# Kernel optimization log

Measured on AMD Instinct MI355X. Metric: run time of the kernel, lower is better.

The kernel has to match this reference:

```python
import jax, jax.numpy as jnp
import numpy as np

N_NODES = 50000
N_EDGES = 800000
N_GRAPHS = 512
IN_DIM = 256
HID = 512
N_CLASSES = 10
BN_EPS = 1e-5


def setup_inputs() -> dict:
    key = jax.random.key(0)
    ks = jax.random.split(key, 32)
    x = jax.random.normal(ks[0], (N_NODES, IN_DIM), dtype=jnp.float32)
    edge_index = jax.random.randint(ks[1], (2, N_EDGES), 0, N_NODES, dtype=jnp.int64)
    batch = jnp.sort(jax.random.randint(ks[2], (N_NODES,), 0, N_GRAPHS, dtype=jnp.int64))

    def lin(k, fan_in, fan_out):
        kw, kb = jax.random.split(k)
        s = 1.0 / np.sqrt(fan_in)
        w = jax.random.uniform(kw, (fan_in, fan_out), jnp.float32, -s, s)
        b = jax.random.uniform(kb, (fan_out,), jnp.float32, -s, s)
        return w, b

    inp = {"x": x, "edge_index": edge_index, "batch": batch}
    # GIN layer 0 MLP (in->hid->hid), layers 1,2 (hid->hid->hid)
    inp["w0a"], inp["b0a"] = lin(ks[3], IN_DIM, HID)
    inp["w0b"], inp["b0b"] = lin(ks[4], HID, HID)
    inp["w1a"], inp["b1a"] = lin(ks[5], HID, HID)
    inp["w1b"], inp["b1b"] = lin(ks[6], HID, HID)
    inp["w2a"], inp["b2a"] = lin(ks[7], HID, HID)
    inp["w2b"], inp["b2b"] = lin(ks[8], HID, HID)
    # BatchNorm affine params
    for i in range(3):
        inp[f"bn{i}_g"] = jnp.ones((HID,), jnp.float32)
        inp[f"bn{i}_b"] = jnp.zeros((HID,), jnp.float32)
    # classifier
    inp["clf_w1"], inp["clf_b1"] = lin(ks[9], HID, HID)
    inp["clf_w2"], inp["clf_b2"] = lin(ks[10], HID, N_CLASSES)
    return inp


def _gin_layer(h, src, dst, wa, ba, wb, bb, g, b):
    # sum-aggregate neighbors (source -> target), eps = 0 (PyG default)
    agg = jax.ops.segment_sum(h[src], dst, num_segments=N_NODES)
    z = h + agg
    # 2-layer MLP: Linear -> ReLU -> Linear
    z = jax.nn.relu(z @ wa + ba) @ wb + bb
    # BatchNorm1d with batch statistics (training mode, biased var) + affine
    mu = jnp.mean(z, axis=0)
    var = jnp.var(z, axis=0)
    z = (z - mu) * jax.lax.rsqrt(var + BN_EPS) * g + b
    return jax.nn.relu(z)


def reference(x, edge_index, batch,
              w0a, b0a, w0b, b0b,
              w1a, b1a, w1b, b1b,
              w2a, b2a, w2b, b2b,
              bn0_g, bn0_b, bn1_g, bn1_b, bn2_g, bn2_b,
              clf_w1, clf_b1, clf_w2, clf_b2):
    src, dst = edge_index[0], edge_index[1]
    h = _gin_layer(x, src, dst, w0a, b0a, w0b, b0b, bn0_g, bn0_b)
    h = _gin_layer(h, src, dst, w1a, b1a, w1b, b1b, bn1_g, bn1_b)
    h = _gin_layer(h, src, dst, w2a, b2a, w2b, b2b, bn2_g, bn2_b)
    # global add pool over graphs
    gpool = jax.ops.segment_sum(h, batch, num_segments=N_GRAPHS)  # [G, HID]
    # classifier (dropout = identity in eval)
    logits = jax.nn.relu(gpool @ clf_w1 + clf_b1) @ clf_w2 + clf_b2
    probs = jax.nn.softmax(logits, axis=1)
    preds = jnp.argmax(probs, axis=1)
    one_hot = jax.nn.one_hot(preds, N_CLASSES, dtype=logits.dtype)
    return (logits, probs, preds.astype(jnp.float32), one_hot)
```

## Files before the change

kernel.cpp:

```cpp
#include <hip/hip_runtime.h>

#define N_NODES 50000
#define N_EDGES 800000
#define N_GRAPHS 512
#define IN_DIM 256
#define HID 512
#define BN_EPS 1e-5f

typedef __attribute__((ext_vector_type(8))) short bf16x8;
typedef __attribute__((ext_vector_type(4))) float f32x4;

__device__ inline void split_bf16(float a, unsigned short& hi, unsigned short& lo) {
  unsigned u = __float_as_uint(a);
  hi = (unsigned short)(u >> 16);
  float fh = __uint_as_float(u & 0xFFFF0000u);
  float r = a - fh;
  lo = (unsigned short)(__float_as_uint(r) >> 16);
}

__device__ inline void split4_store(float4 v, unsigned short* hip, unsigned short* lop) {
  unsigned short h0, h1, h2, h3, l0, l1, l2, l3;
  split_bf16(v.x, h0, l0);
  split_bf16(v.y, h1, l1);
  split_bf16(v.z, h2, l2);
  split_bf16(v.w, h3, l3);
  uint2 hv, lv;
  hv.x = (unsigned)h0 | ((unsigned)h1 << 16);
  hv.y = (unsigned)h2 | ((unsigned)h3 << 16);
  lv.x = (unsigned)l0 | ((unsigned)l1 << 16);
  lv.y = (unsigned)l2 | ((unsigned)l3 << 16);
  *(uint2*)hip = hv;
  *(uint2*)lop = lv;
}

__device__ inline float4 bnrelu4(float4 v, float4 s, float4 h) {
  float4 o;
  o.x = fmaxf(fmaf(v.x, s.x, h.x), 0.f);
  o.y = fmaxf(fmaf(v.y, s.y, h.y), 0.f);
  o.z = fmaxf(fmaf(v.z, s.z, h.z), 0.f);
  o.w = fmaxf(fmaf(v.w, s.w, h.w), 0.f);
  return o;
}

__global__ __launch_bounds__(256) void hist_dst(const int* __restrict__ dst,
                                                int* __restrict__ deg) {
  for (int e = blockIdx.x * 256 + threadIdx.x; e < N_EDGES; e += gridDim.x * 256)
    atomicAdd(&deg[dst[e]], 1);
}

__global__ __launch_bounds__(1024) void scan_deg(const int* __restrict__ deg,
                                                 int* __restrict__ off,
                                                 int* __restrict__ cursor) {
  __shared__ int partial[1024];
  const int t = threadIdx.x;
  const int CHUNK = 49;
  const int base = t * CHUNK;
  int mysum = 0;
  for (int i = 0; i < CHUNK; ++i) {
    int idx = base + i;
    if (idx < N_NODES) mysum += deg[idx];
  }
  partial[t] = mysum;
  __syncthreads();
  for (int st = 1; st < 1024; st <<= 1) {
    int v = (t >= st) ? partial[t - st] : 0;
    __syncthreads();
    partial[t] += v;
    __syncthreads();
  }
  int run = partial[t] - mysum;
  for (int i = 0; i < CHUNK; ++i) {
    int idx = base + i;
    if (idx < N_NODES) {
      off[idx] = run;
      cursor[idx] = run;
      run += deg[idx];
    }
  }
  if (t == 1023) off[N_NODES] = N_EDGES;
}

__global__ __launch_bounds__(256) void fill_csr(const int* __restrict__ src,
                                                const int* __restrict__ dst,
                                                int* __restrict__ cursor,
                                                int* __restrict__ eidx) {
  for (int e = blockIdx.x * 256 + threadIdx.x; e < N_EDGES; e += gridDim.x * 256) {
    int p = atomicAdd(&cursor[dst[e]], 1);
    eidx[p] = src[e];
  }
}

template <int ROWF4, int HASBN>
__global__ __launch_bounds__(256) void agg_pk(const float4* __restrict__ h4,
                                              const int* __restrict__ off,
                                              const int* __restrict__ eidx,
                                              const float4* __restrict__ scale4,
                                              const float4* __restrict__ shift4,
                                              unsigned short* __restrict__ zp) {
  const int n = blockIdx.x * 4 + (threadIdx.x >> 6);
  if (n >= N_NODES) return;
  const int lane = threadIdx.x & 63;
  const int ROW = ROWF4 * 64;
  float4 sc[ROWF4], sh[ROWF4];
  if (HASBN) {
#pragma unroll
    for (int j = 0; j < ROWF4; ++j) {
      sc[j] = scale4[j * 64 + lane];
      sh[j] = shift4[j * 64 + lane];
    }
  }
  float4 v[ROWF4];
  const float4* hn = h4 + (long long)n * ROW;
#pragma unroll
  for (int j = 0; j < ROWF4; ++j) {
    float4 a = hn[j * 64 + lane];
    v[j] = HASBN ? bnrelu4(a, sc[j], sh[j]) : a;
  }

  int p = off[n];
  const int pe = off[n + 1];
  for (; p + 4 <= pe; p += 4) {
    int s0 = eidx[p], s1 = eidx[p + 1], s2 = eidx[p + 2], s3 = eidx[p + 3];
    const float4* h0 = h4 + (long long)s0 * ROW;
    const float4* h1 = h4 + (long long)s1 * ROW;
    const float4* h2 = h4 + (long long)s2 * ROW;
    const float4* h3 = h4 + (long long)s3 * ROW;
#pragma unroll
    for (int j = 0; j < ROWF4; ++j) {
      float4 a = h0[j * 64 + lane];
      float4 b = h1[j * 64 + lane];
      float4 c = h2[j * 64 + lane];
      float4 d = h3[j * 64 + lane];
      if (HASBN) {
        a = bnrelu4(a, sc[j], sh[j]);
        b = bnrelu4(b, sc[j], sh[j]);
        c = bnrelu4(c, sc[j], sh[j]);
        d = bnrelu4(d, sc[j], sh[j]);
      }
      v[j].x += (a.x + b.x) + (c.x + d.x);
      v[j].y += (a.y + b.y) + (c.y + d.y);
      v[j].z += (a.z + b.z) + (c.z + d.z);
      v[j].w += (a.w + b.w) + (c.w + d.w);
    }
  }
  for (; p < pe; ++p) {
    int s0 = eidx[p];
    const float4* h0 = h4 + (long long)s0 * ROW;
#pragma unroll
    for (int j = 0; j < ROWF4; ++j) {
      float4 a = h0[j * 64 + lane];
      if (HASBN) a = bnrelu4(a, sc[j], sh[j]);
      v[j].x += a.x;
      v[j].y += a.y;
      v[j].z += a.z;
      v[j].w += a.w;
    }
  }
  const int nd = n & 63, tile = n >> 6;
  const int nf = nd >> 4, ccs = nd & 15;
#pragma unroll
  for (int j = 0; j < ROWF4; ++j) {
    int cj = j * 64 + lane;
    int ks = cj >> 3, k4 = cj & 7;
    size_t base = ((size_t)tile * (ROWF4 * 8) + ks) * 4096 +
                  (size_t)nf * 512 + (size_t)(k4 >> 1) * 128 + (size_t)ccs * 8 +
                  (size_t)(k4 & 1) * 4;
    split4_store(v[j], zp + base, zp + base + 2048);
  }
}

__global__ __launch_bounds__(256) void wt_build(const float* __restrict__ W,
                                                unsigned short* __restrict__ Wp,
                                                int KS) {
  int gid = blockIdx.x * 256 + threadIdx.x;
  int total = 2 * KS * 8192;
  if (gid >= total) return;
  int blk = gid >> 13;
  int rem = gid & 8191;
  int cf = rem >> 9;
  int q = (rem >> 7) & 3;
  int c = (rem >> 3) & 15;
  int j = rem & 7;
  int bx = blk / KS, ks = blk - bx * KS;
  int chan = bx * 256 + cf * 16 + c;
  int k = ks * 32 + q * 8 + j;
  float v = W[(size_t)k * 512 + chan];
  unsigned short h, l;
  split_bf16(v, h, l);
  Wp[(size_t)blk * 16384 + rem] = h;
  Wp[(size_t)blk * 16384 + 8192 + rem] = l;
}

template <int STATS, int PACKOUT>
__global__ __launch_bounds__(256) void gemm_pk(const unsigned short* __restrict__ Ap,
                                               const unsigned short* __restrict__ Wp,
                                               const float* __restrict__ bias,
                                               float* __restrict__ Cf,
                                               unsigned short* __restrict__ Cp,
                                               float* __restrict__ stat_sum,
                                               float* __restrict__ stat_sq,
                                               int N, int KS, int relu) {
  const int tid = threadIdx.x;
  const int wv = tid >> 6, ln = tid & 63;
  const int bx = blockIdx.x;
  const int tile = blockIdx.y;
  const int n0 = tile * 64;

  f32x4 acc[4][4];
#pragma unroll
  for (int i = 0; i < 4; ++i)
#pragma unroll
    for (int j = 0; j < 4; ++j) acc[i][j] = f32x4{0.f, 0.f, 0.f, 0.f};

  const unsigned short* wp =
      Wp + ((size_t)bx * KS) * 16384 + (size_t)(wv * 4) * 512 + (size_t)ln * 8;
  const unsigned short* ap = Ap + (size_t)tile * KS * 4096 + (size_t)ln * 8;

  for (int ks = 0; ks < KS; ++ks) {
    const unsigned short* w = wp + (size_t)ks * 16384;
    const unsigned short* a = ap + (size_t)ks * 4096;
    bf16x8 wh[4], wl[4], ah[4], al[4];
#pragma unroll
    for (int i = 0; i < 4; ++i) {
      wh[i] = *(const bf16x8*)(w + i * 512);
      wl[i] = *(const bf16x8*)(w + 8192 + i * 512);
    }
#pragma unroll
    for (int j = 0; j < 4; ++j) {
      ah[j] = *(const bf16x8*)(a + j * 512);
      al[j] = *(const bf16x8*)(a + 2048 + j * 512);
    }
#pragma unroll
    for (int i = 0; i < 4; ++i)
#pragma unroll
      for (int j = 0; j < 4; ++j) {
        acc[i][j] = __builtin_amdgcn_mfma_f32_16x16x32_bf16(wh[i], ah[j], acc[i][j], 0, 0, 0);
        acc[i][j] = __builtin_amdgcn_mfma_f32_16x16x32_bf16(wh[i], al[j], acc[i][j], 0, 0, 0);
        acc[i][j] = __builtin_amdgcn_mfma_f32_16x16x32_bf16(wl[i], ah[j], acc[i][j], 0, 0, 0);
      }
  }

  const int chanb = bx * 256 + wv * 64 + (ln >> 4) * 4;
  float4 s4[4], q4[4];
  if (STATS) {
#pragma unroll
    for (int i = 0; i < 4; ++i) {
      s4[i] = make_float4(0.f, 0.f, 0.f, 0.f);
      q4[i] = make_float4(0.f, 0.f, 0.f, 0.f);
    }
  }
#pragma unroll
  for (int j = 0; j < 4; ++j) {
    int node = n0 + j * 16 + (ln & 15);
    bool valid = node < N;
    int nd = node & 63;
    int tile2 = node >> 6, nf = nd >> 4, ccs = nd & 15;
#pragma unroll
    for (int i = 0; i < 4; ++i) {
      int chan = chanb + i * 16;
      float4 bv = *(const float4*)(bias + chan);
      f32x4 a = acc[i][j];
      float4 o;
      o.x = a[0] + bv.x;
      o.y = a[1] + bv.y;
      o.z = a[2] + bv.z;
      o.w = a[3] + bv.w;
      if (relu) {
        o.x = fmaxf(o.x, 0.f);
        o.y = fmaxf(o.y, 0.f);
        o.z = fmaxf(o.z, 0.f);
        o.w = fmaxf(o.w, 0.f);
      }
      if (PACKOUT) {
        if (valid) {
          size_t base = ((size_t)tile2 * 16 + (size_t)(chan >> 5)) * 4096 +
                        (size_t)nf * 512 + (size_t)((chan >> 3) & 3) * 128 +
                        (size_t)ccs * 8 + (size_t)((chan >> 2) & 1) * 4;
          split4_store(o, Cp + base, Cp + base + 2048);
        }
      } else {
        if (valid) *(float4*)(Cf + (size_t)node * 512 + chan) = o;
        if (STATS) {
          if (!valid) o = make_float4(0.f, 0.f, 0.f, 0.f);
          s4[i].x += o.x; s4[i].y += o.y; s4[i].z += o.z; s4[i].w += o.w;
          q4[i].x += o.x * o.x; q4[i].y += o.y * o.y;
          q4[i].z += o.z * o.z; q4[i].w += o.w * o.w;
        }
      }
    }
  }
  if (STATS) {
#pragma unroll
    for (int i = 0; i < 4; ++i) {
#pragma unroll
      for (int mask = 1; mask < 16; mask <<= 1) {
        s4[i].x += __shfl_xor(s4[i].x, mask);
        s4[i].y += __shfl_xor(s4[i].y, mask);
        s4[i].z += __shfl_xor(s4[i].z, mask);
        s4[i].w += __shfl_xor(s4[i].w, mask);
        q4[i].x += __shfl_xor(q4[i].x, mask);
        q4[i].y += __shfl_xor(q4[i].y, mask);
        q4[i].z += __shfl_xor(q4[i].z, mask);
        q4[i].w += __shfl_xor(q4[i].w, mask);
      }
    }
    if ((ln & 15) == 0) {
#pragma unroll
      for (int i = 0; i < 4; ++i) {
        int chan = chanb + i * 16;
        atomicAdd(&stat_sum[chan + 0], s4[i].x);
        atomicAdd(&stat_sum[chan + 1], s4[i].y);
        atomicAdd(&stat_sum[chan + 2], s4[i].z);
        atomicAdd(&stat_sum[chan + 3], s4[i].w);
        atomicAdd(&stat_sq[chan + 0], q4[i].x);
        atomicAdd(&stat_sq[chan + 1], q4[i].y);
        atomicAdd(&stat_sq[chan + 2], q4[i].z);
        atomicAdd(&stat_sq[chan + 3], q4[i].w);
      }
    }
  }
}

__global__ __launch_bounds__(512) void bn_finalize(const float* __restrict__ sum,
                                                   const float* __restrict__ sumsq,
                                                   const float* __restrict__ g,
                                                   const float* __restrict__ b,
                                                   float* __restrict__ scale,
                                                   float* __restrict__ shift) {
  const int c = threadIdx.x;
  const float invN = 1.0f / (float)N_NODES;
  float mu = sum[c] * invN;
  float var = sumsq[c] * invN - mu * mu;
  float sc = rsqrtf(var + BN_EPS) * g[c];
  scale[c] = sc;
  shift[c] = fmaf(-mu, sc, b[c]);
}

__global__ __launch_bounds__(512) void pool_bounds(const int* __restrict__ batch,
                                                   int* __restrict__ gstart) {
  const int g = threadIdx.x;
  int lo = 0, hi = N_NODES;
  while (lo < hi) {
    int mid = (lo + hi) >> 1;
    if (batch[mid] < g) lo = mid + 1;
    else hi = mid;
  }
  gstart[g] = lo;
  if (g == 0) gstart[N_GRAPHS] = N_NODES;
}

__global__ __launch_bounds__(128) void gpool_bn(const float4* __restrict__ z4,
                                                const int* __restrict__ gstart,
                                                const float4* __restrict__ scale4,
                                                const float4* __restrict__ shift4,
                                                unsigned short* __restrict__ gpp) {
  const int g = blockIdx.x;
  const int t = threadIdx.x;
  const int s = gstart[g], e = gstart[g + 1];
  const float4 sc = scale4[t], sh = shift4[t];
  float4 acc = make_float4(0.f, 0.f, 0.f, 0.f);
  for (int n = s; n < e; ++n) {
    float4 v = bnrelu4(z4[(size_t)n * 128 + t], sc, sh);
    acc.x += v.x;
    acc.y += v.y;
    acc.z += v.z;
    acc.w += v.w;
  }
  const int tile = g >> 6, nd = g & 63;
  const int nf = nd >> 4, ccs = nd & 15;
  const int ks = t >> 3, k4 = t & 7;
  size_t base = ((size_t)tile * 16 + ks) * 4096 + (size_t)nf * 512 +
                (size_t)(k4 >> 1) * 128 + (size_t)ccs * 8 + (size_t)(k4 & 1) * 4;
  split4_store(acc, gpp + base, gpp + base + 2048);
}

__global__ __launch_bounds__(64) void clf2_softmax(const float* __restrict__ hidden,
                                                   const float* __restrict__ w2,
                                                   const float* __restrict__ b2,
                                                   float* __restrict__ out) {
  const int g = blockIdx.x;
  const int lane = threadIdx.x;
  float acc[10];
#pragma unroll
  for (int j = 0; j < 10; ++j) acc[j] = 0.f;
  for (int k = lane; k < HID; k += 64) {
    float hv = hidden[(long long)g * HID + k];
#pragma unroll
    for (int j = 0; j < 10; ++j) acc[j] += hv * w2[k * 10 + j];
  }
#pragma unroll
  for (int j = 0; j < 10; ++j) {
    for (int o = 32; o > 0; o >>= 1) acc[j] += __shfl_down(acc[j], o);
  }
  if (lane == 0) {
    float lg[10], pb[10];
    float mx = -1e30f;
#pragma unroll
    for (int j = 0; j < 10; ++j) {
      lg[j] = acc[j] + b2[j];
      mx = fmaxf(mx, lg[j]);
    }
    float se = 0.f;
#pragma unroll
    for (int j = 0; j < 10; ++j) {
      pb[j] = __expf(lg[j] - mx);
      se += pb[j];
    }
    float inv = 1.f / se;
    int am = 0;
    float best = lg[0];
#pragma unroll
    for (int j = 1; j < 10; ++j) {
      if (lg[j] > best) { best = lg[j]; am = j; }
    }
#pragma unroll
    for (int j = 0; j < 10; ++j) out[g * 10 + j] = lg[j];
#pragma unroll
    for (int j = 0; j < 10; ++j) out[N_GRAPHS * 10 + g * 10 + j] = pb[j] * inv;
    out[2 * N_GRAPHS * 10 + g] = (float)am;
#pragma unroll
    for (int j = 0; j < 10; ++j)
      out[2 * N_GRAPHS * 10 + N_GRAPHS + g * 10 + j] = (j == am) ? 1.f : 0.f;
  }
}

extern "C" void kernel_launch(void* const* d_in, const int* in_sizes, int n_in,
                              void* d_out, int out_size, void* d_ws, size_t ws_size,
                              hipStream_t stream) {
  const float* x = (const float*)d_in[0];
  const int* src = (const int*)d_in[1];
  const int* dstE = src + N_EDGES;
  const int* batch = (const int*)d_in[2];
  const float* w0a = (const float*)d_in[3];
  const float* b0a = (const float*)d_in[4];
  const float* w0b = (const float*)d_in[5];
  const float* b0b = (const float*)d_in[6];
  const float* w1a = (const float*)d_in[7];
  const float* b1a = (const float*)d_in[8];
  const float* w1b = (const float*)d_in[9];
  const float* b1b = (const float*)d_in[10];
  const float* w2a = (const float*)d_in[11];
  const float* b2a = (const float*)d_in[12];
  const float* w2b = (const float*)d_in[13];
  const float* b2b = (const float*)d_in[14];
  const float* bng[3] = {(const float*)d_in[15], (const float*)d_in[17], (const float*)d_in[19]};
  const float* bnb[3] = {(const float*)d_in[16], (const float*)d_in[18], (const float*)d_in[20]};
  const float* clf_w1 = (const float*)d_in[21];
  const float* clf_b1 = (const float*)d_in[22];
  const float* clf_w2 = (const float*)d_in[23];
  const float* clf_b2 = (const float*)d_in[24];
  float* out = (float*)d_out;

  const size_t BUF = 25624576;
  float* bufA = (float*)d_ws;
  float* bufB = bufA + BUF;
  float* bnsum = bufB + BUF;
  float* bnsq = bnsum + 512;
  float* scale = bnsq + 512;
  float* shift = scale + 512;
  unsigned short* gpPack = (unsigned short*)(shift + 512);
  float* hidden = (float*)(gpPack + 524288);
  unsigned short* wp0a = (unsigned short*)(hidden + 262144);
  unsigned short* wp0b = wp0a + 262144;
  unsigned short* wp1a = wp0b + 524288;
  unsigned short* wp1b = wp1a + 524288;
  unsigned short* wp2a = wp1b + 524288;
  unsigned short* wp2b = wp2a + 524288;
  unsigned short* wpc1 = wp2b + 524288;
  int* deg = (int*)(wpc1 + 524288);
  int* off = deg + N_NODES;
  int* cursor = off + N_NODES + 1;
  int* eidx = cursor + N_NODES;
  int* gstart = eidx + N_EDGES;

  hipMemsetAsync(deg, 0, N_NODES * sizeof(int), stream);
  hipLaunchKernelGGL(hist_dst, dim3(3125), dim3(256), 0, stream, dstE, deg);
  hipLaunchKernelGGL(scan_deg, dim3(1), dim3(1024), 0, stream, deg, off, cursor);
  hipLaunchKernelGGL(fill_csr, dim3(3125), dim3(256), 0, stream, src, dstE, cursor, eidx);
  hipLaunchKernelGGL(pool_bounds, dim3(1), dim3(512), 0, stream, batch, gstart);

  hipLaunchKernelGGL(wt_build, dim3(512), dim3(256), 0, stream, w0a, wp0a, 8);
  hipLaunchKernelGGL(wt_build, dim3(1024), dim3(256), 0, stream, w0b, wp0b, 16);
  hipLaunchKernelGGL(wt_build, dim3(1024), dim3(256), 0, stream, w1a, wp1a, 16);
  hipLaunchKernelGGL(wt_build, dim3(1024), dim3(256), 0, stream, w1b, wp1b, 16);
  hipLaunchKernelGGL(wt_build, dim3(1024), dim3(256), 0, stream, w2a, wp2a, 16);
  hipLaunchKernelGGL(wt_build, dim3(1024), dim3(256), 0, stream, w2b, wp2b, 16);
  hipLaunchKernelGGL(wt_build, dim3(1024), dim3(256), 0, stream, clf_w1, wpc1, 16);

  const unsigned short* wpa[3] = {wp0a, wp1a, wp2a};
  const unsigned short* wpb[3] = {wp0b, wp1b, wp2b};
  const float* ba[3] = {b0a, b1a, b2a};
  const float* bb[3] = {b0b, b1b, b2b};

  const int NT = (N_NODES + 63) / 64;
  const int nagg = (N_NODES + 3) / 4;

  float* P = bufA;
  float* Q = bufB;
  for (int layer = 0; layer < 3; ++layer) {
    if (layer == 0) {
      hipLaunchKernelGGL((agg_pk<1, 0>), dim3(nagg), dim3(256), 0, stream,
                         (const float4*)x, off, eidx, nullptr, nullptr,
                         (unsigned short*)Q);
    } else {
      hipLaunchKernelGGL((agg_pk<2, 1>), dim3(nagg), dim3(256), 0, stream,
                         (const float4*)P, off, eidx, (const float4*)scale,
                         (const float4*)shift, (unsigned short*)Q);
    }
    { float* t = P; P = Q; Q = t; }
    hipLaunchKernelGGL((gemm_pk<0, 1>), dim3(2, NT), dim3(256), 0, stream,
                       (const unsigned short*)P, wpa[layer], ba[layer],
                       (float*)nullptr, (unsigned short*)Q, nullptr, nullptr,
                       N_NODES, (layer == 0) ? 8 : 16, 1);
    { float* t = P; P = Q; Q = t; }
    hipMemsetAsync(bnsum, 0, 2 * 512 * sizeof(float), stream);
    hipLaunchKernelGGL((gemm_pk<1, 0>), dim3(2, NT), dim3(256), 0, stream,
                       (const unsigned short*)P, wpb[layer], bb[layer],
                       Q, (unsigned short*)nullptr, bnsum, bnsq,
                       N_NODES, 16, 0);
    { float* t = P; P = Q; Q = t; }
    hipLaunchKernelGGL(bn_finalize, dim3(1), dim3(512), 0, stream,
                       bnsum, bnsq, bng[layer], bnb[layer], scale, shift);
  }

  hipLaunchKernelGGL(gpool_bn, dim3(N_GRAPHS), dim3(128), 0, stream,
                     (const float4*)P, gstart, (const float4*)scale,
                     (const float4*)shift, gpPack);
  hipLaunchKernelGGL((gemm_pk<0, 0>), dim3(2, 8), dim3(256), 0, stream,
                     (const unsigned short*)gpPack, wpc1, clf_b1,
                     hidden, (unsigned short*)nullptr, nullptr, nullptr,
                     N_GRAPHS, 16, 1);
  hipLaunchKernelGGL(clf2_softmax, dim3(N_GRAPHS), dim3(64), 0, stream,
                     hidden, clf_w2, clf_b2, out);
}
```

Measured before the change: 1.687 ms.

## Switch activations to row-major split-bf16 layout, double-buffer GEMM loads, widen gather

Replaces the tiled MFMA-fragment packing of activations with a plain row-major layout, storing hi and lo planes at a fixed stride (NTOT rows). The GEMM now reads A rows directly per lane, with KS as a template parameter, a fully unrolled K loop and double-buffered register prefetch of the next K step. The aggregation kernel gathers 8 neighbours per iteration using masked FMAs in place of the 4-wide loop plus scalar tail. Together these aim to add memory-level parallelism and overlap loads with MFMA work, at the cost of less coalesced A loads, more registers per thread, and wasted duplicate loads for padded edges.

```diff
diff --git a/kernel.cpp b/kernel.cpp
--- a/kernel.cpp
+++ b/kernel.cpp
@@ -1,6 +1,7 @@
 #include <hip/hip_runtime.h>
 
 #define N_NODES 50000
+#define NTOT 50048
 #define N_EDGES 800000
 #define N_GRAPHS 512
 #define IN_DIM 256
@@ -101,6 +102,7 @@
   if (n >= N_NODES) return;
   const int lane = threadIdx.x & 63;
   const int ROW = ROWF4 * 64;
+  constexpr size_t ASTR = (size_t)NTOT * (ROWF4 * 256);
   float4 sc[ROWF4], sh[ROWF4];
   if (HASBN) {
 #pragma unroll
@@ -119,53 +121,38 @@
 
   int p = off[n];
   const int pe = off[n + 1];
-  for (; p + 4 <= pe; p += 4) {
-    int s0 = eidx[p], s1 = eidx[p + 1], s2 = eidx[p + 2], s3 = eidx[p + 3];
-    const float4* h0 = h4 + (long long)s0 * ROW;
-    const float4* h1 = h4 + (long long)s1 * ROW;
-    const float4* h2 = h4 + (long long)s2 * ROW;
-    const float4* h3 = h4 + (long long)s3 * ROW;
+  for (; p < pe; p += 8) {
+    const float4* hp[8];
+    float m[8];
+#pragma unroll
+    for (int e = 0; e < 8; ++e) {
+      bool ok = (p + e) < pe;
+      int idx = ok ? (p + e) : (pe - 1);
+      hp[e] = h4 + (long long)eidx[idx] * ROW;
+      m[e] = ok ? 1.f : 0.f;
+    }
 #pragma unroll
     for (int j = 0; j < ROWF4; ++j) {
-      float4 a = h0[j * 64 + lane];
-      float4 b = h1[j * 64 + lane];
-      float4 c = h2[j * 64 + lane];
-      float4 d = h3[j * 64 + lane];
-      if (HASBN) {
-        a = bnrelu4(a, sc[j], sh[j]);
-        b = bnrelu4(b, sc[j], sh[j]);
-        c = bnrelu4(c, sc[j], sh[j]);
-        d = bnrelu4(d, sc[j], sh[j]);
-      }
-      v[j].x += (a.x + b.x) + (c.x + d.x);
-      v[j].y += (a.y + b.y) + (c.y + d.y);
-      v[j].z += (a.z + b.z) + (c.z + d.z);
-      v[j].w += (a.w + b.w) + (c.w + d.w);
-    }
-  }
-  for (; p < pe; ++p) {
-    int s0 = eidx[p];
-    const float4* h0 = h4 + (long long)s0 * ROW;
-#pragma unroll
-    for (int j = 0; j < ROWF4; ++j) {
-      float4 a = h0[j * 64 + lane];
-      if (HASBN) a = bnrelu4(a, sc[j], sh[j]);
-      v[j].x += a.x;
-      v[j].y += a.y;
-      v[j].z += a.z;
-      v[j].w += a.w;
-    }
-  }
-  const int nd = n & 63, tile = n >> 6;
-  const int nf = nd >> 4, ccs = nd & 15;
+      float4 t[8];
+#pragma unroll
+      for (int e = 0; e < 8; ++e) {
+        t[e] = hp[e][j * 64 + lane];
+        if (HASBN) t[e] = bnrelu4(t[e], sc[j], sh[j]);
+      }
+#pragma unroll
+      for (int e = 0; e < 8; ++e) {
+        v[j].x = fmaf(t[e].x, m[e], v[j].x);
+        v[j].y = fmaf(t[e].y, m[e], v[j].y);
+        v[j].z = fmaf(t[e].z, m[e], v[j].z);
+        v[j].w = fmaf(t[e].w, m[e], v[j].w);
+      }
+    }
+  }
+  const size_t nb = (size_t)n * (ROWF4 * 256);
 #pragma unroll
   for (int j = 0; j < ROWF4; ++j) {
-    int cj = j * 64 + lane;
-    int ks = cj >> 3, k4 = cj & 7;
-    size_t base = ((size_t)tile * (ROWF4 * 8) + ks) * 4096 +
-                  (size_t)nf * 512 + (size_t)(k4 >> 1) * 128 + (size_t)ccs * 8 +
-                  (size_t)(k4 & 1) * 4;
-    split4_store(v[j], zp + base, zp + base + 2048);
+    size_t base = nb + (size_t)(j * 64 + lane) * 4;
+    split4_store(v[j], zp + base, zp + ASTR + base);
   }
 }
 
@@ -191,20 +178,24 @@
   Wp[(size_t)blk * 16384 + 8192 + rem] = l;
 }
 
-template <int STATS, int PACKOUT>
-__global__ __launch_bounds__(256) void gemm_pk(const unsigned short* __restrict__ Ap,
+template <int KS, int STATS, int PACKOUT>
+__global__ __launch_bounds__(256) void gemm_nm(const unsigned short* __restrict__ Ap,
+                                               size_t ASTR,
                                                const unsigned short* __restrict__ Wp,
                                                const float* __restrict__ bias,
                                                float* __restrict__ Cf,
                                                unsigned short* __restrict__ Cp,
                                                float* __restrict__ stat_sum,
                                                float* __restrict__ stat_sq,
-                                               int N, int KS, int relu) {
+                                               int N, int relu) {
+  constexpr int K = KS * 32;
+  constexpr size_t CSTR = (size_t)NTOT * 512;
   const int tid = threadIdx.x;
   const int wv = tid >> 6, ln = tid & 63;
   const int bx = blockIdx.x;
   const int tile = blockIdx.y;
   const int n0 = tile * 64;
+  const int q = ln >> 4, ccs = ln & 15;
 
   f32x4 acc[4][4];
 #pragma unroll
@@ -213,32 +204,42 @@
     for (int j = 0; j < 4; ++j) acc[i][j] = f32x4{0.f, 0.f, 0.f, 0.f};
 
   const unsigned short* wp =
-      Wp + ((size_t)bx * KS) * 16384 + (size_t)(wv * 4) * 512 + (size_t)ln * 8;
-  const unsigned short* ap = Ap + (size_t)tile * KS * 4096 + (size_t)ln * 8;
-
+      Wp + (size_t)bx * KS * 16384 + (size_t)(wv * 4) * 512 + (size_t)ln * 8;
+  const unsigned short* aph[4];
+#pragma unroll
+  for (int j = 0; j < 4; ++j)
+    aph[j] = Ap + (size_t)(n0 + j * 16 + ccs) * K + (size_t)q * 8;
+
+  bf16x8 wh[2][4], wl[2][4], ah[2][4], al[2][4];
+
+#define LOADSTG(B, KSI)                                         \
+  {                                                             \
+    const unsigned short* w_ = wp + (size_t)(KSI) * 16384;      \
+    _Pragma("unroll") for (int i_ = 0; i_ < 4; ++i_) {          \
+      wh[B][i_] = *(const bf16x8*)(w_ + i_ * 512);              \
+      wl[B][i_] = *(const bf16x8*)(w_ + 8192 + i_ * 512);       \
+    }                                                           \
+    _Pragma("unroll") for (int j_ = 0; j_ < 4; ++j_) {          \
+      ah[B][j_] = *(const bf16x8*)(aph[j_] + (KSI) * 32);       \
+      al[B][j_] = *(const bf16x8*)(aph[j_] + ASTR + (KSI) * 32);\
+    }                                                           \
+  }
+
+  LOADSTG(0, 0)
+#pragma unroll
   for (int ks = 0; ks < KS; ++ks) {
-    const unsigned short* w = wp + (size_t)ks * 16384;
-    const unsigned short* a = ap + (size_t)ks * 4096;
-    bf16x8 wh[4], wl[4], ah[4], al[4];
-#pragma unroll
-    for (int i = 0; i < 4; ++i) {
-      wh[i] = *(const bf16x8*)(w + i * 512);
-      wl[i] = *(const bf16x8*)(w + 8192 + i * 512);
-    }
-#pragma unroll
-    for (int j = 0; j < 4; ++j) {
-      ah[j] = *(const bf16x8*)(a + j * 512);
-      al[j] = *(const bf16x8*)(a + 2048 + j * 512);
-    }
+    const int cur = ks & 1;
+    if (ks + 1 < KS) LOADSTG(cur ^ 1, ks + 1)
 #pragma unroll
     for (int i = 0; i < 4; ++i)
 #pragma unroll
       for (int j = 0; j < 4; ++j) {
-        acc[i][j] = __builtin_amdgcn_mfma_f32_16x16x32_bf16(wh[i], ah[j], acc[i][j], 0, 0, 0);
-        acc[i][j] = __builtin_amdgcn_mfma_f32_16x16x32_bf16(wh[i], al[j], acc[i][j], 0, 0, 0);
-        acc[i][j] = __builtin_amdgcn_mfma_f32_16x16x32_bf16(wl[i], ah[j], acc[i][j], 0, 0, 0);
-      }
-  }
+        acc[i][j] = __builtin_amdgcn_mfma_f32_16x16x32_bf16(wh[cur][i], ah[cur][j], acc[i][j], 0, 0, 0);
+        acc[i][j] = __builtin_amdgcn_mfma_f32_16x16x32_bf16(wh[cur][i], al[cur][j], acc[i][j], 0, 0, 0);
+        acc[i][j] = __builtin_amdgcn_mfma_f32_16x16x32_bf16(wl[cur][i], ah[cur][j], acc[i][j], 0, 0, 0);
+      }
+  }
+#undef LOADSTG
 
   const int chanb = bx * 256 + wv * 64 + (ln >> 4) * 4;
   float4 s4[4], q4[4];
@@ -253,8 +254,6 @@
   for (int j = 0; j < 4; ++j) {
     int node = n0 + j * 16 + (ln & 15);
     bool valid = node < N;
-    int nd = node & 63;
-    int tile2 = node >> 6, nf = nd >> 4, ccs = nd & 15;
 #pragma unroll
     for (int i = 0; i < 4; ++i) {
       int chan = chanb + i * 16;
@@ -273,10 +272,8 @@
       }
       if (PACKOUT) {
         if (valid) {
-          size_t base = ((size_t)tile2 * 16 + (size_t)(chan >> 5)) * 4096 +
-                        (size_t)nf * 512 + (size_t)((chan >> 3) & 3) * 128 +
-                        (size_t)ccs * 8 + (size_t)((chan >> 2) & 1) * 4;
-          split4_store(o, Cp + base, Cp + base + 2048);
+          size_t base = (size_t)node * 512 + chan;
+          split4_store(o, Cp + base, Cp + CSTR + base);
         }
       } else {
         if (valid) *(float4*)(Cf + (size_t)node * 512 + chan) = o;
@@ -366,12 +363,8 @@
     acc.z += v.z;
     acc.w += v.w;
   }
-  const int tile = g >> 6, nd = g & 63;
-  const int nf = nd >> 4, ccs = nd & 15;
-  const int ks = t >> 3, k4 = t & 7;
-  size_t base = ((size_t)tile * 16 + ks) * 4096 + (size_t)nf * 512 +
-                (size_t)(k4 >> 1) * 128 + (size_t)ccs * 8 + (size_t)(k4 & 1) * 4;
-  split4_store(acc, gpp + base, gpp + base + 2048);
+  size_t base = (size_t)g * 512 + (size_t)t * 4;
+  split4_store(acc, gpp + base, gpp + 262144 + base);
 }
 
 __global__ __launch_bounds__(64) void clf2_softmax(const float* __restrict__ hidden,
@@ -451,7 +444,7 @@
   const float* clf_b2 = (const float*)d_in[24];
   float* out = (float*)d_out;
 
-  const size_t BUF = 25624576;
+  const long long BUF = 25624576LL;
   float* bufA = (float*)d_ws;
   float* bufB = bufA + BUF;
   float* bnsum = bufB + BUF;
@@ -494,6 +487,8 @@
 
   const int NT = (N_NODES + 63) / 64;
   const int nagg = (N_NODES + 3) / 4;
+  const size_t AS256 = (size_t)NTOT * 256;
+  const size_t AS512 = (size_t)NTOT * 512;
 
   float* P = bufA;
   float* Q = bufB;
@@ -508,16 +503,23 @@
                          (const float4*)shift, (unsigned short*)Q);
     }
     { float* t = P; P = Q; Q = t; }
-    hipLaunchKernelGGL((gemm_pk<0, 1>), dim3(2, NT), dim3(256), 0, stream,
-                       (const unsigned short*)P, wpa[layer], ba[layer],
-                       (float*)nullptr, (unsigned short*)Q, nullptr, nullptr,
-                       N_NODES, (layer == 0) ? 8 : 16, 1);
+    if (layer == 0) {
+      hipLaunchKernelGGL((gemm_nm<8, 0, 1>), dim3(2, NT), dim3(256), 0, stream,
+                         (const unsigned short*)P, AS256, wpa[layer], ba[layer],
+                         (float*)nullptr, (unsigned short*)Q, nullptr, nullptr,
+                         N_NODES, 1);
+    } else {
+      hipLaunchKernelGGL((gemm_nm<16, 0, 1>), dim3(2, NT), dim3(256), 0, stream,
+                         (const unsigned short*)P, AS512, wpa[layer], ba[layer],
+                         (float*)nullptr, (unsigned short*)Q, nullptr, nullptr,
+                         N_NODES, 1);
+    }
     { float* t = P; P = Q; Q = t; }
     hipMemsetAsync(bnsum, 0, 2 * 512 * sizeof(float), stream);
-    hipLaunchKernelGGL((gemm_pk<1, 0>), dim3(2, NT), dim3(256), 0, stream,
-                       (const unsigned short*)P, wpb[layer], bb[layer],
+    hipLaunchKernelGGL((gemm_nm<16, 1, 0>), dim3(2, NT), dim3(256), 0, stream,
+                       (const unsigned short*)P, AS512, wpb[layer], bb[layer],
                        Q, (unsigned short*)nullptr, bnsum, bnsq,
-                       N_NODES, 16, 0);
+                       N_NODES, 0);
     { float* t = P; P = Q; Q = t; }
     hipLaunchKernelGGL(bn_finalize, dim3(1), dim3(512), 0, stream,
                        bnsum, bnsq, bng[layer], bnb[layer], scale, shift);
@@ -526,10 +528,10 @@
   hipLaunchKernelGGL(gpool_bn, dim3(N_GRAPHS), dim3(128), 0, stream,
                      (const float4*)P, gstart, (const float4*)scale,
                      (const float4*)shift, gpPack);
-  hipLaunchKernelGGL((gemm_pk<0, 0>), dim3(2, 8), dim3(256), 0, stream,
-                     (const unsigned short*)gpPack, wpc1, clf_b1,
+  hipLaunchKernelGGL((gemm_nm<16, 0, 0>), dim3(2, 8), dim3(256), 0, stream,
+                     (const unsigned short*)gpPack, (size_t)262144, wpc1, clf_b1,
                      hidden, (unsigned short*)nullptr, nullptr, nullptr,
-                     N_GRAPHS, 16, 1);
+                     N_GRAPHS, 1);
   hipLaunchKernelGGL(clf2_softmax, dim3(N_GRAPHS), dim3(64), 0, stream,
                      hidden, clf_w2, clf_b2, out);
 }
```

Measured after the change: 2.037 ms. 1.21x slower.

## Batch edge gathers by eight with masking and simplify packed A-tile layout

Applied to the files above, without the earlier changes.

The neighbor aggregation loop now gathers eight source rows per iteration, using a clamped index and a 0/1 multiplier in place of the separate four-wide and scalar tail loops, so more loads are in flight at once. The packed bf16 hi/lo activation layout is changed to a node-major layout (node*32 + channel within the k-slice), applied consistently to the aggregation writer, the GEMM A-operand reader, the packed GEMM output and the pooled buffer. This gives contiguous stores per node row. It risks wasted loads and FMAs on padded edges for low-degree nodes, and possible LDS-free bank or coalescing changes on the MFMA A loads.

```diff
diff --git a/kernel.cpp b/kernel.cpp
--- a/kernel.cpp
+++ b/kernel.cpp
@@ -119,52 +119,40 @@
 
   int p = off[n];
   const int pe = off[n + 1];
-  for (; p + 4 <= pe; p += 4) {
-    int s0 = eidx[p], s1 = eidx[p + 1], s2 = eidx[p + 2], s3 = eidx[p + 3];
-    const float4* h0 = h4 + (long long)s0 * ROW;
-    const float4* h1 = h4 + (long long)s1 * ROW;
-    const float4* h2 = h4 + (long long)s2 * ROW;
-    const float4* h3 = h4 + (long long)s3 * ROW;
+  for (; p < pe; p += 8) {
+    const float4* hp[8];
+    float m[8];
+#pragma unroll
+    for (int e = 0; e < 8; ++e) {
+      bool ok = (p + e) < pe;
+      int idx = ok ? (p + e) : (pe - 1);
+      hp[e] = h4 + (long long)eidx[idx] * ROW;
+      m[e] = ok ? 1.f : 0.f;
+    }
 #pragma unroll
     for (int j = 0; j < ROWF4; ++j) {
-      float4 a = h0[j * 64 + lane];
-      float4 b = h1[j * 64 + lane];
-      float4 c = h2[j * 64 + lane];
-      float4 d = h3[j * 64 + lane];
-      if (HASBN) {
-        a = bnrelu4(a, sc[j], sh[j]);
-        b = bnrelu4(b, sc[j], sh[j]);
-        c = bnrelu4(c, sc[j], sh[j]);
-        d = bnrelu4(d, sc[j], sh[j]);
-      }
-      v[j].x += (a.x + b.x) + (c.x + d.x);
-      v[j].y += (a.y + b.y) + (c.y + d.y);
-      v[j].z += (a.z + b.z) + (c.z + d.z);
-      v[j].w += (a.w + b.w) + (c.w + d.w);
-    }
-  }
-  for (; p < pe; ++p) {
-    int s0 = eidx[p];
-    const float4* h0 = h4 + (long long)s0 * ROW;
-#pragma unroll
-    for (int j = 0; j < ROWF4; ++j) {
-      float4 a = h0[j * 64 + lane];
-      if (HASBN) a = bnrelu4(a, sc[j], sh[j]);
-      v[j].x += a.x;
-      v[j].y += a.y;
-      v[j].z += a.z;
-      v[j].w += a.w;
+      float4 t[8];
+#pragma unroll
+      for (int e = 0; e < 8; ++e) {
+        t[e] = hp[e][j * 64 + lane];
+        if (HASBN) t[e] = bnrelu4(t[e], sc[j], sh[j]);
+      }
+#pragma unroll
+      for (int e = 0; e < 8; ++e) {
+        v[j].x = fmaf(t[e].x, m[e], v[j].x);
+        v[j].y = fmaf(t[e].y, m[e], v[j].y);
+        v[j].z = fmaf(t[e].z, m[e], v[j].z);
+        v[j].w = fmaf(t[e].w, m[e], v[j].w);
+      }
     }
   }
   const int nd = n & 63, tile = n >> 6;
-  const int nf = nd >> 4, ccs = nd & 15;
 #pragma unroll
   for (int j = 0; j < ROWF4; ++j) {
     int cj = j * 64 + lane;
     int ks = cj >> 3, k4 = cj & 7;
-    size_t base = ((size_t)tile * (ROWF4 * 8) + ks) * 4096 +
-                  (size_t)nf * 512 + (size_t)(k4 >> 1) * 128 + (size_t)ccs * 8 +
-                  (size_t)(k4 & 1) * 4;
+    size_t base = ((size_t)tile * (ROWF4 * 8) + ks) * 4096 + (size_t)nd * 32 +
+                  (size_t)k4 * 4;
     split4_store(v[j], zp + base, zp + base + 2048);
   }
 }
@@ -205,6 +193,7 @@
   const int bx = blockIdx.x;
   const int tile = blockIdx.y;
   const int n0 = tile * 64;
+  const int q = ln >> 4, ccs = ln & 15;
 
   f32x4 acc[4][4];
 #pragma unroll
@@ -214,7 +203,8 @@
 
   const unsigned short* wp =
       Wp + ((size_t)bx * KS) * 16384 + (size_t)(wv * 4) * 512 + (size_t)ln * 8;
-  const unsigned short* ap = Ap + (size_t)tile * KS * 4096 + (size_t)ln * 8;
+  const unsigned short* ap =
+      Ap + (size_t)tile * KS * 4096 + (size_t)ccs * 32 + (size_t)q * 8;
 
   for (int ks = 0; ks < KS; ++ks) {
     const unsigned short* w = wp + (size_t)ks * 16384;
@@ -254,7 +244,7 @@
     int node = n0 + j * 16 + (ln & 15);
     bool valid = node < N;
     int nd = node & 63;
-    int tile2 = node >> 6, nf = nd >> 4, ccs = nd & 15;
+    int tile2 = node >> 6;
 #pragma unroll
     for (int i = 0; i < 4; ++i) {
       int chan = chanb + i * 16;
@@ -274,8 +264,7 @@
       if (PACKOUT) {
         if (valid) {
           size_t base = ((size_t)tile2 * 16 + (size_t)(chan >> 5)) * 4096 +
-                        (size_t)nf * 512 + (size_t)((chan >> 3) & 3) * 128 +
-                        (size_t)ccs * 8 + (size_t)((chan >> 2) & 1) * 4;
+                        (size_t)nd * 32 + (size_t)(chan & 31);
           split4_store(o, Cp + base, Cp + base + 2048);
         }
       } else {
@@ -367,10 +356,8 @@
     acc.w += v.w;
   }
   const int tile = g >> 6, nd = g & 63;
-  const int nf = nd >> 4, ccs = nd & 15;
   const int ks = t >> 3, k4 = t & 7;
-  size_t base = ((size_t)tile * 16 + ks) * 4096 + (size_t)nf * 512 +
-                (size_t)(k4 >> 1) * 128 + (size_t)ccs * 8 + (size_t)(k4 & 1) * 4;
+  size_t base = ((size_t)tile * 16 + ks) * 4096 + (size_t)nd * 32 + (size_t)k4 * 4;
   split4_store(acc, gpp + base, gpp + base + 2048);
 }
 
@@ -451,7 +438,7 @@
   const float* clf_b2 = (const float*)d_in[24];
   float* out = (float*)d_out;
 
-  const size_t BUF = 25624576;
+  const long long BUF = 25624576LL;
   float* bufA = (float*)d_ws;
   float* bufB = bufA + BUF;
   float* bnsum = bufB + BUF;
```

Measured after the change: 1.668 ms. No clear change (-1.1%).
